# Optimization experiments

Hardware: AMD Instinct MI355X
Metric: run time of the kernel (lower is better)

## Reference

```python
import jax, jax.numpy as jnp
import numpy as np
from jax import lax

B, C, H, W = 2, 384, 32, 32
N_HEAD, N_GROUP = 12, 6
HC = C // N_HEAD          # 32 head channels
GC = C // N_GROUP         # 64 group channels
GH = N_HEAD // N_GROUP    # 2 heads per group
KK = 7                    # depthwise kernel (25<=32<=48)
OFF_FACTOR = 2.0
SCALE = HC ** -0.5
EPS = 1e-5


def setup_inputs() -> dict:
    key = jax.random.key(0)
    ks = jax.random.split(key, 16)
    s = 0.02
    inp = {
        "x": jax.random.normal(ks[0], (B, C, H, W), jnp.float32),
        "Wq": jax.random.normal(ks[1], (C, C), jnp.float32) * s,
        "bq": jnp.zeros((C,), jnp.float32),
        "Wk": jax.random.normal(ks[2], (C, C), jnp.float32) * s,
        "bk": jnp.zeros((C,), jnp.float32),
        "Wv": jax.random.normal(ks[3], (C, C), jnp.float32) * s,
        "bv": jnp.zeros((C,), jnp.float32),
        "Wo": jax.random.normal(ks[4], (C, C), jnp.float32) * s,
        "bo": jnp.zeros((C,), jnp.float32),
        "off_dw_w": jax.random.normal(ks[5], (GC, 1, KK, KK), jnp.float32) * s,  # depthwise OIHW
        "off_dw_b": jnp.zeros((GC,), jnp.float32),
        "ln_g": jnp.ones((GC,), jnp.float32),
        "ln_b": jnp.zeros((GC,), jnp.float32),
        "off_pw_w": jax.random.normal(ks[6], (2, GC), jnp.float32) * s,  # 1x1 conv, no bias
        "rpe_table": jax.random.normal(ks[7], (N_HEAD, 2 * H - 1, 2 * W - 1), jnp.float32) * 0.01,
    }
    return inp


def _ref_points(Hk, Wk):
    # torch.linspace(0.5, Hk-0.5, Hk)/Hk*2-1 == ((i+0.5)/Hk)*2-1
    ry = ((jnp.arange(Hk, dtype=jnp.float32) + 0.5) / Hk) * 2.0 - 1.0
    rx = ((jnp.arange(Wk, dtype=jnp.float32) + 0.5) / Wk) * 2.0 - 1.0
    gy, gx = jnp.meshgrid(ry, rx, indexing='ij')
    return jnp.stack((gy, gx), axis=-1)  # [Hk, Wk, 2] in (y, x) order


def _grid_sample(img, grid):
    # img: [N, Cc, Hi, Wi]; grid: [N, Hg, Wg, 2] in (x, y), align_corners=True, zeros padding
    N, Cc, Hi, Wi = img.shape
    Hg, Wg = grid.shape[1], grid.shape[2]
    gx = (grid[..., 0] + 1.0) * 0.5 * (Wi - 1)
    gy = (grid[..., 1] + 1.0) * 0.5 * (Hi - 1)
    x0 = jnp.floor(gx)
    y0 = jnp.floor(gy)
    wx = gx - x0
    wy = gy - y0
    img_f = img.reshape(N, Cc, Hi * Wi)

    def corner(xi, yi, w):
        valid = (xi >= 0) & (xi <= Wi - 1) & (yi >= 0) & (yi <= Hi - 1)
        xc = jnp.clip(xi, 0, Wi - 1).astype(jnp.int32)
        yc = jnp.clip(yi, 0, Hi - 1).astype(jnp.int32)
        idx = (yc * Wi + xc).reshape(N, 1, Hg * Wg)
        vals = jnp.take_along_axis(img_f, jnp.broadcast_to(idx, (N, Cc, Hg * Wg)), axis=2)
        w = (w * valid.astype(img.dtype)).reshape(N, 1, Hg * Wg)
        return vals * w

    out = (corner(x0, y0, (1 - wx) * (1 - wy))
           + corner(x0 + 1, y0, wx * (1 - wy))
           + corner(x0, y0 + 1, (1 - wx) * wy)
           + corner(x0 + 1, y0 + 1, wx * wy))
    return out.reshape(N, Cc, Hg, Wg)


def _conv1x1(x, w, b=None):
    y = jnp.einsum('bchw,oc->bohw', x, w)
    if b is not None:
        y = y + b[None, :, None, None]
    return y


def _forward(x, Wq, bq, Wk, bk, Wv, bv, Wo, bo, off_dw_w, off_dw_b, ln_g, ln_b, off_pw_w, rpe_table):
    q = _conv1x1(x, Wq, bq)                                        # [B, C, H, W]
    q_off = q.reshape(B * N_GROUP, GC, H, W)
    # conv_offset: depthwise conv -> LayerNorm(ch) -> GELU -> 1x1 conv to 2 ch
    o = lax.conv_general_dilated(q_off, off_dw_w, (1, 1), ((KK // 2, KK // 2), (KK // 2, KK // 2)),
                                 feature_group_count=GC,
                                 dimension_numbers=('NCHW', 'OIHW', 'NCHW'))
    o = o + off_dw_b[None, :, None, None]
    mu = jnp.mean(o, axis=1, keepdims=True)
    var = jnp.mean((o - mu) ** 2, axis=1, keepdims=True)
    o = (o - mu) * lax.rsqrt(var + EPS) * ln_g[None, :, None, None] + ln_b[None, :, None, None]
    o = jax.nn.gelu(o, approximate=False)
    off = jnp.einsum('bchw,oc->bohw', o, off_pw_w)                 # [BG, 2, Hs, Ws]
    Hs, Ws = off.shape[2], off.shape[3]
    n_sample = Hs * Ws
    off_range = jnp.array([1.0 / Hs, 1.0 / Ws], jnp.float32).reshape(1, 2, 1, 1)
    off = jnp.tanh(off) * off_range * OFF_FACTOR
    off = jnp.transpose(off, (0, 2, 3, 1))                         # [BG, Hs, Ws, 2] (y, x)
    pos = off + _ref_points(Hs, Ws)[None]                          # [BG, Hs, Ws, 2]

    x_g = x.reshape(B * N_GROUP, GC, H, W)
    x_s = _grid_sample(x_g, pos[..., ::-1])                        # [BG, GC, Hs, Ws]
    x_s = x_s.reshape(B, C, 1, n_sample)

    k = _conv1x1(x_s, Wk, bk).reshape(B * N_HEAD, HC, n_sample)
    v = _conv1x1(x_s, Wv, bv).reshape(B * N_HEAD, HC, n_sample)
    qh = q.reshape(B * N_HEAD, HC, H * W)
    attn = jnp.einsum('bcm,bcn->bmn', qh, k) * SCALE               # [BH, HW, ns]

    # RPE: bilinear lookup of relative-position table at query-sample displacements
    q_grid = _ref_points(H, W).reshape(1, H * W, 1, 2)
    disp = (q_grid - pos.reshape(B * N_GROUP, 1, n_sample, 2)) * 0.5  # [BG, HW, ns, 2] (y, x)
    rpe_b = jnp.broadcast_to(rpe_table[None], (B, N_HEAD, 2 * H - 1, 2 * W - 1))
    rpe_b = rpe_b.reshape(B * N_GROUP, GH, 2 * H - 1, 2 * W - 1)
    attn_bias = _grid_sample(rpe_b, disp[..., ::-1])               # [BG, GH, HW, ns]
    attn = attn + attn_bias.reshape(B * N_HEAD, H * W, n_sample)

    attn = jax.nn.softmax(attn, axis=2)
    out = jnp.einsum('bmn,bcn->bcm', attn, v).reshape(B, C, H, W)
    y = _conv1x1(out, Wo, bo)
    return y


def reference(x, Wq, bq, Wk, bk, Wv, bv, Wo, bo, off_dw_w, off_dw_b, ln_g, ln_b, off_pw_w, rpe_table):
    return _forward(x, Wq, bq, Wk, bk, Wv, bv, Wo, bo,
                    off_dw_w, off_dw_b, ln_g, ln_b, off_pw_w, rpe_table)
```

## Files before the change

### kernel.cpp

```cpp
#include <hip/hip_runtime.h>
#include <hip/hip_fp16.h>
#include <math.h>

#define HH 32
#define WW 32
#define HWSZ 1024
#define CC 384
#define NHEAD 12
#define NGROUP 6
#define HC 32
#define GC 64
#define NS 1024
#define ATTN_SCALE 0.17677669529663687f

typedef _Float16 half8_t __attribute__((ext_vector_type(8)));
typedef _Float16 half4_t __attribute__((ext_vector_type(4)));
typedef _Float16 half2_t __attribute__((ext_vector_type(2)));
typedef float    f4_t    __attribute__((ext_vector_type(4)));

template<int XLO>
__global__ __launch_bounds__(256) void gemm_wx(
    const float* __restrict__ W, const float* __restrict__ bias,
    const float* __restrict__ X, float* __restrict__ Y)
{
    const int bz = blockIdx.z;
    const int tm = blockIdx.y * 32;
    const int tn = blockIdx.x * 64;
    const int tid = threadIdx.x;
    const int w = tid >> 6, lane = tid & 63;
    const int quad = lane >> 4, lcol = lane & 15;

    __shared__ _Float16 sWh[32][40];
    __shared__ _Float16 sXh[64][40];
    __shared__ _Float16 sXl[XLO ? 64 : 1][40];

    const float* Xb = X + (size_t)bz * CC * 1024;
    float* Yb = Y + (size_t)bz * CC * 1024;

    f4_t acc0 = {0.f, 0.f, 0.f, 0.f}, acc1 = {0.f, 0.f, 0.f, 0.f};

    for (int k0 = 0; k0 < CC; k0 += 32) {
        {
            int m = tid >> 3, k4 = (tid & 7) * 4;
            float4 wv = *(const float4*)&W[(size_t)(tm + m) * CC + k0 + k4];
            half4_t h; h[0] = (_Float16)wv.x; h[1] = (_Float16)wv.y;
            h[2] = (_Float16)wv.z; h[3] = (_Float16)wv.w;
            *(half4_t*)&sWh[m][k4] = h;
        }
        {
            int k = tid >> 3, nj = tid & 7;
            const float* xr = &Xb[(size_t)(k0 + k) * 1024 + tn + nj];
#pragma unroll
            for (int i = 0; i < 8; ++i) {
                float v = xr[8 * i];
                _Float16 h = (_Float16)v;
                sXh[nj + 8 * i][k] = h;
                if (XLO) sXl[nj + 8 * i][k] = (_Float16)(v - (float)h);
            }
        }
        __syncthreads();

        half8_t Ah0 = *(const half8_t*)&sWh[lcol][quad * 8];
        half8_t Ah1 = *(const half8_t*)&sWh[16 + lcol][quad * 8];
        half8_t Bh  = *(const half8_t*)&sXh[w * 16 + lcol][quad * 8];
        acc0 = __builtin_amdgcn_mfma_f32_16x16x32_f16(Ah0, Bh, acc0, 0, 0, 0);
        acc1 = __builtin_amdgcn_mfma_f32_16x16x32_f16(Ah1, Bh, acc1, 0, 0, 0);
        if (XLO) {
            half8_t Bl = *(const half8_t*)&sXl[w * 16 + lcol][quad * 8];
            acc0 = __builtin_amdgcn_mfma_f32_16x16x32_f16(Ah0, Bl, acc0, 0, 0, 0);
            acc1 = __builtin_amdgcn_mfma_f32_16x16x32_f16(Ah1, Bl, acc1, 0, 0, 0);
        }
        __syncthreads();
    }

#pragma unroll
    for (int r = 0; r < 4; ++r) {
        int m0 = tm + quad * 4 + r;
        Yb[(size_t)m0 * 1024 + tn + w * 16 + lcol]        = acc0[r] + bias[m0];
        Yb[(size_t)(m0 + 16) * 1024 + tn + w * 16 + lcol] = acc1[r] + bias[m0 + 16];
    }
}

__global__ __launch_bounds__(256) void gemm_kv_fused(
    const float* __restrict__ Wk, const float* __restrict__ bk,
    const float* __restrict__ Wv, const float* __restrict__ bv,
    const _Float16* __restrict__ X,
    _Float16* __restrict__ khT, _Float16* __restrict__ vhb)
{
    const int bz = blockIdx.z;
    const int head = blockIdx.y;
    const int tm = head * 32;
    const int tn = blockIdx.x * 64;
    const int tid = threadIdx.x;
    const int w = tid >> 6, lane = tid & 63;
    const int quad = lane >> 4, lcol = lane & 15;
    const int bh = bz * 12 + head;

    __shared__ _Float16 sWk[32][40], sWv[32][40];
    __shared__ _Float16 sXh[64][40];

    const _Float16* Xb = X + (size_t)bz * CC * 1024;

    f4_t ak0 = {0.f, 0.f, 0.f, 0.f}, ak1 = {0.f, 0.f, 0.f, 0.f};
    f4_t av0 = {0.f, 0.f, 0.f, 0.f}, av1 = {0.f, 0.f, 0.f, 0.f};

    for (int k0 = 0; k0 < CC; k0 += 32) {
        {
            int m = tid >> 3, k4 = (tid & 7) * 4;
            float4 wk = *(const float4*)&Wk[(size_t)(tm + m) * CC + k0 + k4];
            float4 wv = *(const float4*)&Wv[(size_t)(tm + m) * CC + k0 + k4];
            half4_t hk; hk[0] = (_Float16)wk.x; hk[1] = (_Float16)wk.y;
            hk[2] = (_Float16)wk.z; hk[3] = (_Float16)wk.w;
            half4_t hv; hv[0] = (_Float16)wv.x; hv[1] = (_Float16)wv.y;
            hv[2] = (_Float16)wv.z; hv[3] = (_Float16)wv.w;
            *(half4_t*)&sWk[m][k4] = hk;
            *(half4_t*)&sWv[m][k4] = hv;
        }
        {
            int k = tid >> 3, nj = (tid & 7) * 8;
            half8_t hv = *(const half8_t*)&Xb[(size_t)(k0 + k) * 1024 + tn + nj];
#pragma unroll
            for (int i = 0; i < 8; ++i)
                sXh[nj + i][k] = hv[i];
        }
        __syncthreads();

        half8_t Xa = *(const half8_t*)&sXh[w * 16 + lcol][quad * 8];
        half8_t K0 = *(const half8_t*)&sWk[lcol][quad * 8];
        half8_t K1 = *(const half8_t*)&sWk[16 + lcol][quad * 8];
        half8_t V0 = *(const half8_t*)&sWv[lcol][quad * 8];
        half8_t V1 = *(const half8_t*)&sWv[16 + lcol][quad * 8];
        ak0 = __builtin_amdgcn_mfma_f32_16x16x32_f16(Xa, K0, ak0, 0, 0, 0);
        ak1 = __builtin_amdgcn_mfma_f32_16x16x32_f16(Xa, K1, ak1, 0, 0, 0);
        av0 = __builtin_amdgcn_mfma_f32_16x16x32_f16(V0, Xa, av0, 0, 0, 0);
        av1 = __builtin_amdgcn_mfma_f32_16x16x32_f16(V1, Xa, av1, 0, 0, 0);
        __syncthreads();
    }

    {
        float bk0 = bk[tm + lcol], bk1 = bk[tm + 16 + lcol];
#pragma unroll
        for (int r = 0; r < 4; ++r) {
            int n = tn + w * 16 + quad * 4 + r;
            khT[((size_t)bh * 1024 + n) * 32 + lcol]      = (_Float16)(ak0[r] + bk0);
            khT[((size_t)bh * 1024 + n) * 32 + 16 + lcol] = (_Float16)(ak1[r] + bk1);
        }
    }
    {
#pragma unroll
        for (int r = 0; r < 4; ++r) {
            int hc0 = quad * 4 + r;
            vhb[((size_t)bh * 32 + hc0) * 1024 + tn + w * 16 + lcol] =
                (_Float16)(av0[r] + bv[tm + hc0]);
            vhb[((size_t)bh * 32 + hc0 + 16) * 1024 + tn + w * 16 + lcol] =
                (_Float16)(av1[r] + bv[tm + hc0 + 16]);
        }
    }
}

__global__ __launch_bounds__(256) void dwconv_kernel(
    const float* __restrict__ q, const float* __restrict__ dww,
    const float* __restrict__ dwb, float* __restrict__ oconv)
{
    const int bc = blockIdx.x;
    const int bg = bc >> 6, c = bc & 63;
    const int b = bg / 6, g = bg % 6;
    const float* plane = q + ((size_t)b * CC + g * 64 + c) * 1024;

    __shared__ float sp[1024];
    __shared__ float sw[49];
    const int tid = threadIdx.x;
    for (int i = tid; i < 1024; i += 256) sp[i] = plane[i];
    if (tid < 49) sw[tid] = dww[c * 49 + tid];
    __syncthreads();

    const float bias = dwb[c];
    for (int i = tid; i < 1024; i += 256) {
        int y = i >> 5, x = i & 31;
        float s = 0.f;
#pragma unroll
        for (int ky = 0; ky < 7; ++ky) {
            int yy = y + ky - 3;
            if (yy < 0 || yy > 31) continue;
#pragma unroll
            for (int kx = 0; kx < 7; ++kx) {
                int xx = x + kx - 3;
                if (xx < 0 || xx > 31) continue;
                s += sp[yy * 32 + xx] * sw[ky * 7 + kx];
            }
        }
        oconv[(size_t)bc * 1024 + i] = s + bias;
    }
}

__global__ __launch_bounds__(256) void offset_sample_once_kernel(
    const float* __restrict__ oconv, const float* __restrict__ lng,
    const float* __restrict__ lnb, const float* __restrict__ pw,
    const float* __restrict__ x, float* __restrict__ pos,
    _Float16* __restrict__ xs)
{
    const int bg = blockIdx.y;
    const int px0 = blockIdx.x * 64;
    const int t = threadIdx.x;
    const int cg = t >> 6, pl = t & 63;
    const int px = px0 + pl;
    const int b = bg / 6, g = bg % 6;

    __shared__ float red[4][64];
    __shared__ float spos[64][2];

    const float* base = oconv + ((size_t)bg * 64 + cg * 16) * 1024 + px;
    float col[16];
    float s = 0.f;
#pragma unroll
    for (int i = 0; i < 16; ++i) { col[i] = base[(size_t)i * 1024]; s += col[i]; }
    red[cg][pl] = s;
    __syncthreads();
    float mu = (red[0][pl] + red[1][pl] + red[2][pl] + red[3][pl]) * (1.f / 64.f);
    float v = 0.f;
#pragma unroll
    for (int i = 0; i < 16; ++i) { float d = col[i] - mu; v += d * d; }
    __syncthreads();
    red[cg][pl] = v;
    __syncthreads();
    float inv = rsqrtf((red[0][pl] + red[1][pl] + red[2][pl] + red[3][pl]) * (1.f / 64.f) + 1e-5f);

    float oy = 0.f, ox = 0.f;
#pragma unroll
    for (int i = 0; i < 16; ++i) {
        int c = cg * 16 + i;
        float val = (col[i] - mu) * inv * lng[c] + lnb[c];
        float gl = 0.5f * val * (1.f + erff(val * 0.70710678118654752440f));
        oy += gl * pw[c];
        ox += gl * pw[64 + c];
    }
    __syncthreads();
    red[cg][pl] = oy;
    __syncthreads();
    float oyt = red[0][pl] + red[1][pl] + red[2][pl] + red[3][pl];
    __syncthreads();
    red[cg][pl] = ox;
    __syncthreads();
    if (cg == 0) {
        float oxt = red[0][pl] + red[1][pl] + red[2][pl] + red[3][pl];
        float offy = tanhf(oyt) * (2.0f / 32.0f);
        float offx = tanhf(oxt) * (2.0f / 32.0f);
        int y = px >> 5, xx = px & 31;
        float ry = ((y + 0.5f) / 32.f) * 2.f - 1.f;
        float rx = ((xx + 0.5f) / 32.f) * 2.f - 1.f;
        float pyv = offy + ry, pxv = offx + rx;
        spos[pl][0] = pyv; spos[pl][1] = pxv;
        pos[((size_t)bg * 1024 + px) * 2 + 0] = pyv;
        pos[((size_t)bg * 1024 + px) * 2 + 1] = pxv;
    }
    __syncthreads();

    float py = spos[pl][0], pxv = spos[pl][1];
    float gx = (pxv + 1.f) * 0.5f * 31.f;
    float gy = (py + 1.f) * 0.5f * 31.f;
    float x0f = floorf(gx), y0f = floorf(gy);
    float wx = gx - x0f, wy = gy - y0f;
    int x0 = (int)x0f, y0 = (int)y0f;
    float vx0 = ((unsigned)x0 <= 31u) ? 1.f : 0.f;
    float vx1 = ((unsigned)(x0 + 1) <= 31u) ? 1.f : 0.f;
    float vy0 = ((unsigned)y0 <= 31u) ? 1.f : 0.f;
    float vy1 = ((unsigned)(y0 + 1) <= 31u) ? 1.f : 0.f;
    float w00 = (1.f - wx) * (1.f - wy) * vx0 * vy0;
    float w01 = wx * (1.f - wy) * vx1 * vy0;
    float w10 = (1.f - wx) * wy * vx0 * vy1;
    float w11 = wx * wy * vx1 * vy1;
    int xc0 = min(max(x0, 0), 31), xc1 = min(max(x0 + 1, 0), 31);
    int yc0 = min(max(y0, 0), 31), yc1 = min(max(y0 + 1, 0), 31);
    int i00 = yc0 * 32 + xc0, i01 = yc0 * 32 + xc1;
    int i10 = yc1 * 32 + xc0, i11 = yc1 * 32 + xc1;

    const float* xg = x + ((size_t)b * CC + g * 64) * 1024;
    _Float16* xso = xs + ((size_t)b * CC + g * 64) * 1024 + px;
#pragma unroll
    for (int cs = 0; cs < 4; ++cs) {
        int c0 = cs * 16 + cg * 4;
#pragma unroll
        for (int i = 0; i < 4; ++i) {
            const float* plane = xg + (size_t)(c0 + i) * 1024;
            xso[(size_t)(c0 + i) * 1024] =
                (_Float16)(plane[i00] * w00 + plane[i01] * w01
                         + plane[i10] * w10 + plane[i11] * w11);
        }
    }
}

__global__ __launch_bounds__(256) void attn_mfma_kernel(
    const float* __restrict__ q, const _Float16* __restrict__ khT,
    const _Float16* __restrict__ vhb, const float* __restrict__ pos,
    const float* __restrict__ rpe, float* __restrict__ out)
{
    const int bgp = blockIdx.y;
    const int b = bgp / 6, g = bgp % 6;
    const int h0 = g * 2;
    const int bh0 = b * 12 + h0, bh1 = bh0 + 1;
    const int mblk = blockIdx.x * 16;
    const int tid = threadIdx.x;
    const int w = tid >> 6, lane = tid & 63;
    const int quad = lane >> 4, lcol = lane & 15;

    __shared__ __align__(16) char smem[50944];
    half2_t*  srpeA = (half2_t*)smem;
    half2_t*  srpeB = (half2_t*)(smem + 8832);
    _Float16* sqh   = (_Float16*)(smem + 17664);
    _Float16* spw   = (_Float16*)(smem + 19712) + w * 2304;
    float*    cml0  = (float*)(smem + 38144);
    float*    cml1  = (float*)(smem + 38400);
    float2*   skxy  = (float2*)(smem + 38656);
    int*      siy   = (int*)(smem + 46848);
    float*    comb0 = (float*)(smem + 19712);
    float*    comb1 = (float*)(smem + 19712 + 9216);

    const float qyw = (((mblk >> 5) + 0.5f) * (1.f / 32.f)) * 2.f - 1.f;
    int r0; {
        float gy_lo = (qyw - 1.03125f) * 15.5f + 31.f;
        r0 = (int)floorf(gy_lo);
        r0 = min(max(r0, 0), 28);
    }

    {
        const float* rp0 = rpe + (size_t)h0 * 3969;
        const float* rp1 = rp0 + 3969;
        for (int i = tid; i < 35 * 63; i += 256) {
            int y = i / 63, xx = i - y * 63;
            int gi = (r0 + y) * 63 + xx;
            float a0 = rp0[gi], b0 = (xx < 62) ? rp0[gi + 1] : 0.f;
            float a1 = rp1[gi], b1 = (xx < 62) ? rp1[gi + 1] : 0.f;
            half2_t hA; hA[0] = (_Float16)a0; hA[1] = (_Float16)a1;
            half2_t hB; hB[0] = (_Float16)b0; hB[1] = (_Float16)b1;
            srpeA[i] = hA;
            srpeB[i] = hB;
        }
    }
    {
        const float* qb = q + ((size_t)b * CC + h0 * 32) * 1024 + mblk;
        for (int i = tid; i < 1024; i += 256) {
            int hh = i >> 9, rem = i & 511;
            int hc = rem >> 4, m = rem & 15;
            sqh[hh * 512 + m * 32 + hc] =
                (_Float16)qb[(size_t)(hh * 32 + hc) * 1024 + m];
        }
    }
    {
        const float2* pgv = (const float2*)(pos + (size_t)bgp * 2048);
        for (int i = tid; i < 1024; i += 256) {
            float2 pp = pgv[i];
            float gy = (qyw - pp.x) * 15.5f + 31.f;
            float y0f = floorf(gy);
            skxy[i] = make_float2(pp.y, gy - y0f);
            siy[i] = ((int)y0f - r0) * 63;
        }
    }
    __syncthreads();

    half8_t qf0 = *(const half8_t*)&sqh[lcol * 32 + quad * 8];
    half8_t qf1 = *(const half8_t*)&sqh[512 + lcol * 32 + quad * 8];
    const float qx = (((mblk & 31) + lcol + 0.5f) * (1.f / 32.f)) * 2.f - 1.f;

    const _Float16* khb0 = khT + (size_t)bh0 * 1024 * 32;
    const _Float16* khb1 = khT + (size_t)bh1 * 1024 * 32;
    const _Float16* vhh0 = vhb + (size_t)bh0 * 32 * 1024;
    const _Float16* vhh1 = vhb + (size_t)bh1 * 32 * 1024;

    f4_t o00 = {0.f, 0.f, 0.f, 0.f}, o01 = {0.f, 0.f, 0.f, 0.f};
    f4_t o10 = {0.f, 0.f, 0.f, 0.f}, o11 = {0.f, 0.f, 0.f, 0.f};
    float lsum0 = 0.f, lsum1 = 0.f;

#pragma unroll 1
    for (int c = 0; c < 4; ++c) {
        const int n0 = w * 256 + c * 64;

        half8_t khv0[4], khv1[4];
#pragma unroll
        for (int t = 0; t < 4; ++t) {
            size_t off = (size_t)(n0 + t * 16 + lcol) * 32 + quad * 8;
            khv0[t] = *(const half8_t*)&khb0[off];
            khv1[t] = *(const half8_t*)&khb1[off];
        }

        f4_t S0[4], S1[4];
#pragma unroll
        for (int t = 0; t < 4; ++t) {
            f4_t s0 = {0.f, 0.f, 0.f, 0.f}, s1 = {0.f, 0.f, 0.f, 0.f};
            s0 = __builtin_amdgcn_mfma_f32_16x16x32_f16(khv0[t], qf0, s0, 0, 0, 0);
            s1 = __builtin_amdgcn_mfma_f32_16x16x32_f16(khv1[t], qf1, s1, 0, 0, 0);
#pragma unroll
            for (int r = 0; r < 4; ++r) {
                int key = n0 + t * 16 + quad * 4 + r;
                float2 kxy = skxy[key];
                int iy = siy[key];
                float gx = (qx - kxy.x) * 15.5f + 31.f;
                float x0f = floorf(gx);
                float wxf = gx - x0f;
                int i00 = iy + (int)x0f;
                half2_t a0 = srpeA[i00];
                half2_t b0 = srpeB[i00];
                half2_t a1 = srpeA[i00 + 63];
                half2_t b1 = srpeB[i00 + 63];
                _Float16 wxs = (_Float16)wxf;
                _Float16 wys = (_Float16)kxy.y;
                half2_t wxh; wxh[0] = wxs; wxh[1] = wxs;
                half2_t wyh; wyh[0] = wys; wyh[1] = wys;
                half2_t top = a0 + (b0 - a0) * wxh;
                half2_t bot = a1 + (b1 - a1) * wxh;
                half2_t res = top + (bot - top) * wyh;
                s0[r] = s0[r] * ATTN_SCALE + (float)res[0];
                s1[r] = s1[r] * ATTN_SCALE + (float)res[1];
            }
            S0[t] = s0; S1[t] = s1;
        }

        half8_t vv00[2], vv01[2];
#pragma unroll
        for (int kp = 0; kp < 2; ++kp) {
            int nb = n0 + kp * 32 + quad * 8;
            vv00[kp] = *(const half8_t*)&vhh0[(size_t)lcol * 1024 + nb];
            vv01[kp] = *(const half8_t*)&vhh0[(size_t)(16 + lcol) * 1024 + nb];
        }

#pragma unroll
        for (int t = 0; t < 4; ++t) {
            float p0 = __expf(S0[t][0]), p1 = __expf(S0[t][1]);
            float p2 = __expf(S0[t][2]), p3 = __expf(S0[t][3]);
            lsum0 += (p0 + p1) + (p2 + p3);
            half4_t h;
            h[0] = (_Float16)p0; h[1] = (_Float16)p1;
            h[2] = (_Float16)p2; h[3] = (_Float16)p3;
            *(half4_t*)&spw[lcol * 72 + t * 16 + quad * 4] = h;
            float r0e = __expf(S1[t][0]), r1e = __expf(S1[t][1]);
            float r2e = __expf(S1[t][2]), r3e = __expf(S1[t][3]);
            lsum1 += (r0e + r1e) + (r2e + r3e);
            half4_t h1;
            h1[0] = (_Float16)r0e; h1[1] = (_Float16)r1e;
            h1[2] = (_Float16)r2e; h1[3] = (_Float16)r3e;
            *(half4_t*)&spw[1152 + lcol * 72 + t * 16 + quad * 4] = h1;
        }

#pragma unroll
        for (int kp = 0; kp < 2; ++kp) {
            half8_t pb = *(const half8_t*)&spw[lcol * 72 + kp * 32 + quad * 8];
            o00 = __builtin_amdgcn_mfma_f32_16x16x32_f16(vv00[kp], pb, o00, 0, 0, 0);
            o01 = __builtin_amdgcn_mfma_f32_16x16x32_f16(vv01[kp], pb, o01, 0, 0, 0);
        }
#pragma unroll
        for (int kp = 0; kp < 2; ++kp) {
            int nb = n0 + kp * 32 + quad * 8;
            half8_t v0 = *(const half8_t*)&vhh1[(size_t)lcol * 1024 + nb];
            half8_t v1 = *(const half8_t*)&vhh1[(size_t)(16 + lcol) * 1024 + nb];
            half8_t pb = *(const half8_t*)&spw[1152 + lcol * 72 + kp * 32 + quad * 8];
            o10 = __builtin_amdgcn_mfma_f32_16x16x32_f16(v0, pb, o10, 0, 0, 0);
            o11 = __builtin_amdgcn_mfma_f32_16x16x32_f16(v1, pb, o11, 0, 0, 0);
        }
    }

    lsum0 += __shfl_xor(lsum0, 16); lsum0 += __shfl_xor(lsum0, 32);
    lsum1 += __shfl_xor(lsum1, 16); lsum1 += __shfl_xor(lsum1, 32);

    __syncthreads();

    *(f4_t*)&comb0[(w * 16 + lcol) * 36 + quad * 4]      = o00;
    *(f4_t*)&comb0[(w * 16 + lcol) * 36 + 16 + quad * 4] = o01;
    *(f4_t*)&comb1[(w * 16 + lcol) * 36 + quad * 4]      = o10;
    *(f4_t*)&comb1[(w * 16 + lcol) * 36 + 16 + quad * 4] = o11;
    if (quad == 0) {
        cml0[w * 16 + lcol] = lsum0;
        cml1[w * 16 + lcol] = lsum1;
    }
    __syncthreads();

#pragma unroll
    for (int i = 0; i < 2; ++i) {
        int idx = tid + i * 256;
        int qq = idx >> 5, hc = idx & 31;
        {
            float L = cml0[qq] + cml0[16 + qq] + cml0[32 + qq] + cml0[48 + qq];
            float o = comb0[(0 * 16 + qq) * 36 + hc]
                    + comb0[(1 * 16 + qq) * 36 + hc]
                    + comb0[(2 * 16 + qq) * 36 + hc]
                    + comb0[(3 * 16 + qq) * 36 + hc];
            out[((size_t)b * CC + h0 * 32 + hc) * 1024 + mblk + qq] = o / L;
        }
        {
            float L = cml1[qq] + cml1[16 + qq] + cml1[32 + qq] + cml1[48 + qq];
            float o = comb1[(0 * 16 + qq) * 36 + hc]
                    + comb1[(1 * 16 + qq) * 36 + hc]
                    + comb1[(2 * 16 + qq) * 36 + hc]
                    + comb1[(3 * 16 + qq) * 36 + hc];
            out[((size_t)b * CC + (h0 + 1) * 32 + hc) * 1024 + mblk + qq] = o / L;
        }
    }
}

extern "C" void kernel_launch(void* const* d_in, const int* in_sizes, int n_in,
                              void* d_out, int out_size, void* d_ws, size_t ws_size,
                              hipStream_t stream) {
    const float* x   = (const float*)d_in[0];
    const float* Wq  = (const float*)d_in[1];
    const float* bq  = (const float*)d_in[2];
    const float* Wk  = (const float*)d_in[3];
    const float* bk  = (const float*)d_in[4];
    const float* Wv  = (const float*)d_in[5];
    const float* bv  = (const float*)d_in[6];
    const float* Wo  = (const float*)d_in[7];
    const float* bo  = (const float*)d_in[8];
    const float* dww = (const float*)d_in[9];
    const float* dwb = (const float*)d_in[10];
    const float* lng = (const float*)d_in[11];
    const float* lnb = (const float*)d_in[12];
    const float* pw  = (const float*)d_in[13];
    const float* rpe = (const float*)d_in[14];

    float* ws = (float*)d_ws;
    const size_t SZ = 786432;
    float* qbuf  = ws;
    _Float16* xs = (_Float16*)(ws + 1 * SZ);
    float* abuf  = ws + 2 * SZ;
    float* oconv = ws + 3 * SZ;
    _Float16* khT = (_Float16*)(ws + 4 * SZ);
    _Float16* vhb = (_Float16*)(ws + 5 * SZ);
    float* pos   = ws + 6 * SZ;

    dim3 gqo(16, 12, 2);
    gemm_wx<0><<<gqo, 256, 0, stream>>>(Wq, bq, x, qbuf);
    dwconv_kernel<<<768, 256, 0, stream>>>(qbuf, dww, dwb, oconv);
    offset_sample_once_kernel<<<dim3(16, 12), 256, 0, stream>>>(
        oconv, lng, lnb, pw, x, pos, xs);
    gemm_kv_fused<<<dim3(16, 12, 2), 256, 0, stream>>>(Wk, bk, Wv, bv, xs, khT, vhb);
    attn_mfma_kernel<<<dim3(64, 12), 256, 0, stream>>>(qbuf, khT, vhb, pos, rpe, abuf);
    gemm_wx<1><<<gqo, 256, 0, stream>>>(Wo, bo, abuf, (float*)d_out);
}
```

Measured before the change: 163.0 us.

## Halve GEMM N-tile, split warps across tiles, and register-prefetch next K slice

Both projection GEMMs shrink their N tile from 64 to 32 columns, doubling the grid to 768 blocks. Each warp now owns one 16x16 output tile, or in the fused KV kernel either the K or the V half. The next K-slice of weights and activations is loaded into registers before the MFMA, so global latency overlaps compute. The aim is more blocks on the many CUs and hidden load latency, at the cost of more redundant weight loads and half the MFMA work per sync.

Result: faster. 158.4 us (-2.9%).

```diff
diff --git a/kernel.cpp b/kernel.cpp
--- a/kernel.cpp
+++ b/kernel.cpp
@@ -25,59 +25,62 @@
 {
     const int bz = blockIdx.z;
     const int tm = blockIdx.y * 32;
-    const int tn = blockIdx.x * 64;
+    const int tn = blockIdx.x * 32;
     const int tid = threadIdx.x;
     const int w = tid >> 6, lane = tid & 63;
     const int quad = lane >> 4, lcol = lane & 15;
-
-    __shared__ _Float16 sWh[32][40];
-    __shared__ _Float16 sXh[64][40];
-    __shared__ _Float16 sXl[XLO ? 64 : 1][40];
+    const int wr = w >> 1, wc = w & 1;
+
+    __shared__ _Float16 sW[32][40];
+    __shared__ _Float16 sX[32][40];
+    __shared__ _Float16 sXl[XLO ? 32 : 1][40];
 
     const float* Xb = X + (size_t)bz * CC * 1024;
     float* Yb = Y + (size_t)bz * CC * 1024;
 
-    f4_t acc0 = {0.f, 0.f, 0.f, 0.f}, acc1 = {0.f, 0.f, 0.f, 0.f};
-
+    const int m  = tid >> 3;
+    const int j4 = (tid & 7) * 4;
+
+    float4 wv = *(const float4*)&W[(size_t)(tm + m) * CC + j4];
+    float4 xv = *(const float4*)&Xb[(size_t)m * 1024 + tn + j4];
+
+    f4_t acc = {0.f, 0.f, 0.f, 0.f};
+
+#pragma unroll 1
     for (int k0 = 0; k0 < CC; k0 += 32) {
         {
-            int m = tid >> 3, k4 = (tid & 7) * 4;
-            float4 wv = *(const float4*)&W[(size_t)(tm + m) * CC + k0 + k4];
-            half4_t h; h[0] = (_Float16)wv.x; h[1] = (_Float16)wv.y;
-            h[2] = (_Float16)wv.z; h[3] = (_Float16)wv.w;
-            *(half4_t*)&sWh[m][k4] = h;
-        }
-        {
-            int k = tid >> 3, nj = tid & 7;
-            const float* xr = &Xb[(size_t)(k0 + k) * 1024 + tn + nj];
-#pragma unroll
-            for (int i = 0; i < 8; ++i) {
-                float v = xr[8 * i];
+            half4_t hw; hw[0] = (_Float16)wv.x; hw[1] = (_Float16)wv.y;
+            hw[2] = (_Float16)wv.z; hw[3] = (_Float16)wv.w;
+            *(half4_t*)&sW[m][j4] = hw;
+#pragma unroll
+            for (int i = 0; i < 4; ++i) {
+                float v = (i == 0) ? xv.x : (i == 1) ? xv.y : (i == 2) ? xv.z : xv.w;
                 _Float16 h = (_Float16)v;
-                sXh[nj + 8 * i][k] = h;
-                if (XLO) sXl[nj + 8 * i][k] = (_Float16)(v - (float)h);
+                sX[j4 + i][m] = h;
+                if (XLO) sXl[j4 + i][m] = (_Float16)(v - (float)h);
             }
         }
         __syncthreads();
 
-        half8_t Ah0 = *(const half8_t*)&sWh[lcol][quad * 8];
-        half8_t Ah1 = *(const half8_t*)&sWh[16 + lcol][quad * 8];
-        half8_t Bh  = *(const half8_t*)&sXh[w * 16 + lcol][quad * 8];
-        acc0 = __builtin_amdgcn_mfma_f32_16x16x32_f16(Ah0, Bh, acc0, 0, 0, 0);
-        acc1 = __builtin_amdgcn_mfma_f32_16x16x32_f16(Ah1, Bh, acc1, 0, 0, 0);
+        if (k0 + 32 < CC) {
+            wv = *(const float4*)&W[(size_t)(tm + m) * CC + k0 + 32 + j4];
+            xv = *(const float4*)&Xb[(size_t)(k0 + 32 + m) * 1024 + tn + j4];
+        }
+
+        half8_t A = *(const half8_t*)&sW[wr * 16 + lcol][quad * 8];
+        half8_t B = *(const half8_t*)&sX[wc * 16 + lcol][quad * 8];
+        acc = __builtin_amdgcn_mfma_f32_16x16x32_f16(A, B, acc, 0, 0, 0);
         if (XLO) {
-            half8_t Bl = *(const half8_t*)&sXl[w * 16 + lcol][quad * 8];
-            acc0 = __builtin_amdgcn_mfma_f32_16x16x32_f16(Ah0, Bl, acc0, 0, 0, 0);
-            acc1 = __builtin_amdgcn_mfma_f32_16x16x32_f16(Ah1, Bl, acc1, 0, 0, 0);
+            half8_t Bl = *(const half8_t*)&sXl[wc * 16 + lcol][quad * 8];
+            acc = __builtin_amdgcn_mfma_f32_16x16x32_f16(A, Bl, acc, 0, 0, 0);
         }
         __syncthreads();
     }
 
 #pragma unroll
     for (int r = 0; r < 4; ++r) {
-        int m0 = tm + quad * 4 + r;
-        Yb[(size_t)m0 * 1024 + tn + w * 16 + lcol]        = acc0[r] + bias[m0];
-        Yb[(size_t)(m0 + 16) * 1024 + tn + w * 16 + lcol] = acc1[r] + bias[m0 + 16];
+        int m0 = tm + wr * 16 + quad * 4 + r;
+        Yb[(size_t)m0 * 1024 + tn + wc * 16 + lcol] = acc[r] + bias[m0];
     }
 }
 
@@ -90,70 +93,79 @@
     const int bz = blockIdx.z;
     const int head = blockIdx.y;
     const int tm = head * 32;
-    const int tn = blockIdx.x * 64;
+    const int tn = blockIdx.x * 32;
     const int tid = threadIdx.x;
     const int w = tid >> 6, lane = tid & 63;
     const int quad = lane >> 4, lcol = lane & 15;
     const int bh = bz * 12 + head;
+    const int nt = w & 1;
 
     __shared__ _Float16 sWk[32][40], sWv[32][40];
-    __shared__ _Float16 sXh[64][40];
+    __shared__ _Float16 sX[32][40];
 
     const _Float16* Xb = X + (size_t)bz * CC * 1024;
 
-    f4_t ak0 = {0.f, 0.f, 0.f, 0.f}, ak1 = {0.f, 0.f, 0.f, 0.f};
-    f4_t av0 = {0.f, 0.f, 0.f, 0.f}, av1 = {0.f, 0.f, 0.f, 0.f};
-
+    const int m  = tid >> 3;
+    const int j4 = (tid & 7) * 4;
+
+    float4 wkv = *(const float4*)&Wk[(size_t)(tm + m) * CC + j4];
+    float4 wvv = *(const float4*)&Wv[(size_t)(tm + m) * CC + j4];
+    half4_t xh = *(const half4_t*)&Xb[(size_t)m * 1024 + tn + j4];
+
+    f4_t a0 = {0.f, 0.f, 0.f, 0.f}, a1 = {0.f, 0.f, 0.f, 0.f};
+
+#pragma unroll 1
     for (int k0 = 0; k0 < CC; k0 += 32) {
         {
-            int m = tid >> 3, k4 = (tid & 7) * 4;
-            float4 wk = *(const float4*)&Wk[(size_t)(tm + m) * CC + k0 + k4];
-            float4 wv = *(const float4*)&Wv[(size_t)(tm + m) * CC + k0 + k4];
-            half4_t hk; hk[0] = (_Float16)wk.x; hk[1] = (_Float16)wk.y;
-            hk[2] = (_Float16)wk.z; hk[3] = (_Float16)wk.w;
-            half4_t hv; hv[0] = (_Float16)wv.x; hv[1] = (_Float16)wv.y;
-            hv[2] = (_Float16)wv.z; hv[3] = (_Float16)wv.w;
-            *(half4_t*)&sWk[m][k4] = hk;
-            *(half4_t*)&sWv[m][k4] = hv;
-        }
-        {
-            int k = tid >> 3, nj = (tid & 7) * 8;
-            half8_t hv = *(const half8_t*)&Xb[(size_t)(k0 + k) * 1024 + tn + nj];
-#pragma unroll
-            for (int i = 0; i < 8; ++i)
-                sXh[nj + i][k] = hv[i];
+            half4_t hk; hk[0] = (_Float16)wkv.x; hk[1] = (_Float16)wkv.y;
+            hk[2] = (_Float16)wkv.z; hk[3] = (_Float16)wkv.w;
+            half4_t hv; hv[0] = (_Float16)wvv.x; hv[1] = (_Float16)wvv.y;
+            hv[2] = (_Float16)wvv.z; hv[3] = (_Float16)wvv.w;
+            *(half4_t*)&sWk[m][j4] = hk;
+            *(half4_t*)&sWv[m][j4] = hv;
+#pragma unroll
+            for (int i = 0; i < 4; ++i)
+                sX[j4 + i][m] = xh[i];
         }
         __syncthreads();
 
-        half8_t Xa = *(const half8_t*)&sXh[w * 16 + lcol][quad * 8];
-        half8_t K0 = *(const half8_t*)&sWk[lcol][quad * 8];
-        half8_t K1 = *(const half8_t*)&sWk[16 + lcol][quad * 8];
-        half8_t V0 = *(const half8_t*)&sWv[lcol][quad * 8];
-        half8_t V1 = *(const half8_t*)&sWv[16 + lcol][quad * 8];
-        ak0 = __builtin_amdgcn_mfma_f32_16x16x32_f16(Xa, K0, ak0, 0, 0, 0);
-        ak1 = __builtin_amdgcn_mfma_f32_16x16x32_f16(Xa, K1, ak1, 0, 0, 0);
-        av0 = __builtin_amdgcn_mfma_f32_16x16x32_f16(V0, Xa, av0, 0, 0, 0);
-        av1 = __builtin_amdgcn_mfma_f32_16x16x32_f16(V1, Xa, av1, 0, 0, 0);
+        if (k0 + 32 < CC) {
+            wkv = *(const float4*)&Wk[(size_t)(tm + m) * CC + k0 + 32 + j4];
+            wvv = *(const float4*)&Wv[(size_t)(tm + m) * CC + k0 + 32 + j4];
+            xh  = *(const half4_t*)&Xb[(size_t)(k0 + 32 + m) * 1024 + tn + j4];
+        }
+
+        half8_t Xa = *(const half8_t*)&sX[nt * 16 + lcol][quad * 8];
+        if (w < 2) {
+            half8_t K0 = *(const half8_t*)&sWk[lcol][quad * 8];
+            half8_t K1 = *(const half8_t*)&sWk[16 + lcol][quad * 8];
+            a0 = __builtin_amdgcn_mfma_f32_16x16x32_f16(Xa, K0, a0, 0, 0, 0);
+            a1 = __builtin_amdgcn_mfma_f32_16x16x32_f16(Xa, K1, a1, 0, 0, 0);
+        } else {
+            half8_t V0 = *(const half8_t*)&sWv[lcol][quad * 8];
+            half8_t V1 = *(const half8_t*)&sWv[16 + lcol][quad * 8];
+            a0 = __builtin_amdgcn_mfma_f32_16x16x32_f16(V0, Xa, a0, 0, 0, 0);
+            a1 = __builtin_amdgcn_mfma_f32_16x16x32_f16(V1, Xa, a1, 0, 0, 0);
+        }
         __syncthreads();
     }
 
-    {
+    if (w < 2) {
         float bk0 = bk[tm + lcol], bk1 = bk[tm + 16 + lcol];
 #pragma unroll
         for (int r = 0; r < 4; ++r) {
-            int n = tn + w * 16 + quad * 4 + r;
-            khT[((size_t)bh * 1024 + n) * 32 + lcol]      = (_Float16)(ak0[r] + bk0);
-            khT[((size_t)bh * 1024 + n) * 32 + 16 + lcol] = (_Float16)(ak1[r] + bk1);
-        }
-    }
-    {
+            int n = tn + nt * 16 + quad * 4 + r;
+            khT[((size_t)bh * 1024 + n) * 32 + lcol]      = (_Float16)(a0[r] + bk0);
+            khT[((size_t)bh * 1024 + n) * 32 + 16 + lcol] = (_Float16)(a1[r] + bk1);
+        }
+    } else {
 #pragma unroll
         for (int r = 0; r < 4; ++r) {
             int hc0 = quad * 4 + r;
-            vhb[((size_t)bh * 32 + hc0) * 1024 + tn + w * 16 + lcol] =
-                (_Float16)(av0[r] + bv[tm + hc0]);
-            vhb[((size_t)bh * 32 + hc0 + 16) * 1024 + tn + w * 16 + lcol] =
-                (_Float16)(av1[r] + bv[tm + hc0 + 16]);
+            vhb[((size_t)bh * 32 + hc0) * 1024 + tn + nt * 16 + lcol] =
+                (_Float16)(a0[r] + bv[tm + hc0]);
+            vhb[((size_t)bh * 32 + hc0 + 16) * 1024 + tn + nt * 16 + lcol] =
+                (_Float16)(a1[r] + bv[tm + hc0 + 16]);
         }
     }
 }
@@ -524,12 +536,12 @@
     _Float16* vhb = (_Float16*)(ws + 5 * SZ);
     float* pos   = ws + 6 * SZ;
 
-    dim3 gqo(16, 12, 2);
+    dim3 gqo(32, 12, 2);
     gemm_wx<0><<<gqo, 256, 0, stream>>>(Wq, bq, x, qbuf);
     dwconv_kernel<<<768, 256, 0, stream>>>(qbuf, dww, dwb, oconv);
     offset_sample_once_kernel<<<dim3(16, 12), 256, 0, stream>>>(
         oconv, lng, lnb, pw, x, pos, xs);
-    gemm_kv_fused<<<dim3(16, 12, 2), 256, 0, stream>>>(Wk, bk, Wv, bv, xs, khT, vhb);
+    gemm_kv_fused<<<dim3(32, 12, 2), 256, 0, stream>>>(Wk, bk, Wv, bv, xs, khT, vhb);
     attn_mfma_kernel<<<dim3(64, 12), 256, 0, stream>>>(qbuf, khT, vhb, pos, rpe, abuf);
     gemm_wx<1><<<gqo, 256, 0, stream>>>(Wo, bo, abuf, (float*)d_out);
 }
```
